# Kernel tuning notes

Hardware: AMD Instinct MI355X
Metric: run time of the kernel (lower is better)

The kernel has to match this reference:

```python
import jax, jax.numpy as jnp
import numpy as np

P_DROP = 0.2
N_NODES = 100000
N_EDGES = 1600000
IN_DIM, HID_DIM, OUT_DIM = 128, 128, 64


def sage_conv(x, src, dst, Wl, Wr, b, n_nodes):
    # PyG SAGEConv (aggr='mean', root_weight=True):
    #   out_i = W_l @ mean_{j in N(i)} x_j + W_r @ x_i + b
    msgs = jnp.take(x, src, axis=0)                                   # [E, d]
    agg = jax.ops.segment_sum(msgs, dst, num_segments=n_nodes)        # [N, d]
    cnt = jax.ops.segment_sum(jnp.ones((src.shape[0],), x.dtype), dst,
                              num_segments=n_nodes)                   # [N]
    agg = agg / jnp.maximum(cnt, 1.0)[:, None]                        # mean, 0 for isolated nodes
    return agg @ Wl + x @ Wr + b


def setup_inputs() -> dict:
    key = jax.random.key(0)
    ks = jax.random.split(key, 8)
    x = jax.random.normal(ks[0], (N_NODES, IN_DIM), dtype=jnp.float32)
    edge_index = jax.random.randint(ks[1], (2, N_EDGES), 0, N_NODES, dtype=jnp.int32)
    drop_u = jax.random.uniform(ks[2], (N_NODES, HID_DIM), dtype=jnp.float32)
    s1 = 1.0 / np.sqrt(IN_DIM)
    s2 = 1.0 / np.sqrt(HID_DIM)
    W1l = jax.random.normal(ks[3], (IN_DIM, HID_DIM), dtype=jnp.float32) * s1
    W1r = jax.random.normal(ks[4], (IN_DIM, HID_DIM), dtype=jnp.float32) * s1
    b1 = jnp.zeros((HID_DIM,), dtype=jnp.float32)
    W2l = jax.random.normal(ks[5], (HID_DIM, OUT_DIM), dtype=jnp.float32) * s2
    W2r = jax.random.normal(ks[6], (HID_DIM, OUT_DIM), dtype=jnp.float32) * s2
    b2 = jnp.zeros((OUT_DIM,), dtype=jnp.float32)
    return {"x": x, "edge_index": edge_index, "drop_u": drop_u,
            "W1l": W1l, "W1r": W1r, "b1": b1,
            "W2l": W2l, "W2r": W2r, "b2": b2}


def reference(x, edge_index, drop_u, W1l, W1r, b1, W2l, W2r, b2):
    n = x.shape[0]
    src, dst = edge_index[0], edge_index[1]
    h = jax.nn.elu(sage_conv(x, src, dst, W1l, W1r, b1, n))
    keep = (drop_u >= P_DROP).astype(h.dtype) / (1.0 - P_DROP)  # inverted dropout, p=0.2
    h = h * keep
    h = jax.nn.elu(sage_conv(h, src, dst, W2l, W2r, b2, n))
    return h
```

## Files before the change

kernel.cpp:

```cpp
#include <hip/hip_runtime.h>
#include <cstdint>
#include <cstddef>

#define TPB 256
#define BCAP 2560
#define NBKMAX 800
#define EPB 8192

typedef short bf16x8 __attribute__((ext_vector_type(8)));
typedef float f32x4 __attribute__((ext_vector_type(4)));

__device__ __forceinline__ unsigned short f2bf(float f) {
  unsigned int u = __float_as_uint(f);
  unsigned int r = (u + 0x7fffu + ((u >> 16) & 1u)) >> 16;
  return (unsigned short)r;
}
__device__ __forceinline__ float bf2f(unsigned short h) {
  return __uint_as_float(((unsigned int)h) << 16);
}

__device__ __forceinline__ void gload16(const void* g, void* l) {
  __builtin_amdgcn_global_load_lds(
      (const __attribute__((address_space(1))) unsigned int*)g,
      (__attribute__((address_space(3))) unsigned int*)l, 16, 0, 0);
}


__global__ __launch_bounds__(256) void multisplit_scatter(
    const int* __restrict__ src, const int* __restrict__ dst,
    unsigned int* __restrict__ be, int* __restrict__ bcnt, int e, int nbk) {
  __shared__ int hist[NBKMAX];
  __shared__ int curs[NBKMAX];
  int tx = threadIdx.x;
  int e0 = blockIdx.x * EPB;
  int e1 = min(e, e0 + EPB);

  for (int b = tx; b < nbk; b += TPB) hist[b] = 0;
  __syncthreads();
  for (int i = e0 + tx; i < e1; i += TPB) atomicAdd(&hist[dst[i] >> 7], 1);
  __syncthreads();
  int rot = (blockIdx.x * 131) % nbk;
  for (int s = tx; s < nbk; s += TPB) {
    int b = s + rot;
    if (b >= nbk) b -= nbk;
    int h = hist[b];
    curs[b] = (h > 0) ? atomicAdd(&bcnt[b], h) : 0;
  }
  __syncthreads();
  for (int i = e0 + tx; i < e1; i += TPB) {
    int d = dst[i];
    int b = d >> 7;
    int p = atomicAdd(&curs[b], 1);
    if (p < BCAP)
      be[(size_t)b * BCAP + p] = ((unsigned int)(d & 127) << 17) | (unsigned int)src[i];
  }
}

__global__ void bucket_scan(const int* __restrict__ bcnt, int* __restrict__ bbase, int nbk) {
  __shared__ int s[TPB];
  __shared__ int carry;
  int tx = threadIdx.x;
  if (tx == 0) carry = 0;
  __syncthreads();
  for (int base = 0; base < nbk; base += TPB) {
    int i = base + tx;
    int v = (i < nbk) ? bcnt[i] : 0;
    s[tx] = v;
    __syncthreads();
    for (int d = 1; d < TPB; d <<= 1) {
      int t = (tx >= d) ? s[tx - d] : 0;
      __syncthreads();
      s[tx] += t;
      __syncthreads();
    }
    int c = carry;
    if (i < nbk) bbase[i] = c + s[tx] - v;
    __syncthreads();
    if (tx == TPB - 1) carry = c + s[tx];
    __syncthreads();
  }
}

__global__ __launch_bounds__(256) void per_bucket_build(
    const unsigned int* __restrict__ be, const int* __restrict__ bcnt,
    const int* __restrict__ bbase, int* __restrict__ off, int* __restrict__ col,
    int n, int e) {
  int b = blockIdx.x, tx = threadIdx.x;
  int cnt = bcnt[b];
  if (cnt > BCAP) cnt = BCAP;
  int base = bbase[b];
  int node0 = b << 7;
  __shared__ int scnt[128];
  __shared__ int sscan[128];
  if (tx < 128) scnt[tx] = 0;
  __syncthreads();
  const unsigned int* eb = be + (size_t)b * BCAP;
  for (int i = tx; i < cnt; i += 256) atomicAdd(&scnt[eb[i] >> 17], 1);
  __syncthreads();
  if (tx < 128) sscan[tx] = scnt[tx];
  __syncthreads();
  for (int d = 1; d < 128; d <<= 1) {
    int t = 0;
    if (tx < 128 && tx >= d) t = sscan[tx - d];
    __syncthreads();
    if (tx < 128) sscan[tx] += t;
    __syncthreads();
  }
  if (tx < 128) {
    int excl = sscan[tx] - scnt[tx];
    if (node0 + tx < n) off[node0 + tx] = base + excl;
    scnt[tx] = excl;
  }
  if (b == 0 && tx == 0) off[n] = e;
  __syncthreads();
  for (int i = tx; i < cnt; i += 256) {
    unsigned int u = eb[i];
    int p = atomicAdd(&scnt[u >> 17], 1);
    col[base + p] = (int)(u & 0x1ffff);
  }
}


__global__ void f32_to_bf16_v4(const float* __restrict__ in, unsigned short* __restrict__ out,
                               int n4) {
  int i = blockIdx.x * TPB + threadIdx.x;
  if (i >= n4) return;
  float4 v = ((const float4*)in)[i];
  ushort4 o;
  o.x = f2bf(v.x); o.y = f2bf(v.y); o.z = f2bf(v.z); o.w = f2bf(v.w);
  ((ushort4*)out)[i] = o;
}

__global__ void make_dropmask(const float* __restrict__ u, unsigned char* __restrict__ m,
                              int n4) {
  int i = blockIdx.x * TPB + threadIdx.x;
  if (i >= n4) return;
  float4 v = ((const float4*)u)[i];
  uchar4 o;
  o.x = (v.x >= 0.2f) ? 1 : 0;
  o.y = (v.y >= 0.2f) ? 1 : 0;
  o.z = (v.z >= 0.2f) ? 1 : 0;
  o.w = (v.w >= 0.2f) ? 1 : 0;
  ((uchar4*)m)[i] = o;
}

template <int NF>
__global__ void build_wt(const float* __restrict__ Wl, const float* __restrict__ Wr,
                         unsigned short* __restrict__ Wt) {
  int idx = blockIdx.x * TPB + threadIdx.x;
  if (idx >= NF * 256) return;
  int nn = idx >> 8;
  int k = idx & 255;
  float v = (k < 128) ? Wl[k * NF + nn] : Wr[(k - 128) * NF + nn];
  Wt[idx] = f2bf(v);
}


__global__ void aggregate_bf(const unsigned short* __restrict__ X,
                             const int* __restrict__ off, const int* __restrict__ col,
                             unsigned short* __restrict__ out, int n) {
  int node = (blockIdx.x * TPB + threadIdx.x) >> 6;
  int lane = threadIdx.x & 63;
  if (node >= n) return;
  int s0 = off[node], s1 = off[node + 1];
  float ax = 0.f, ay = 0.f;
  int e = s0;
  for (; e + 4 <= s1; e += 4) {
    int c0 = col[e], c1 = col[e + 1], c2 = col[e + 2], c3 = col[e + 3];
    unsigned int v0 = *(const unsigned int*)(X + (size_t)c0 * 128 + lane * 2);
    unsigned int v1 = *(const unsigned int*)(X + (size_t)c1 * 128 + lane * 2);
    unsigned int v2 = *(const unsigned int*)(X + (size_t)c2 * 128 + lane * 2);
    unsigned int v3 = *(const unsigned int*)(X + (size_t)c3 * 128 + lane * 2);
    ax += bf2f(v0 & 0xffff) + bf2f(v1 & 0xffff) + bf2f(v2 & 0xffff) + bf2f(v3 & 0xffff);
    ay += bf2f(v0 >> 16) + bf2f(v1 >> 16) + bf2f(v2 >> 16) + bf2f(v3 >> 16);
  }
  for (; e < s1; ++e) {
    int c = col[e];
    unsigned int v = *(const unsigned int*)(X + (size_t)c * 128 + lane * 2);
    ax += bf2f(v & 0xffff);
    ay += bf2f(v >> 16);
  }
  float inv = (s1 > s0) ? 1.0f / (float)(s1 - s0) : 0.f;
  unsigned int o = ((unsigned int)f2bf(ay * inv) << 16) | f2bf(ax * inv);
  *(unsigned int*)(out + (size_t)node * 128 + lane * 2) = o;
}


template <int NT, bool DROP, bool OUT32>
__global__ __launch_bounds__(256) void gemm_mfma(
    const unsigned short* __restrict__ A1, const unsigned short* __restrict__ A2,
    const unsigned short* __restrict__ Wt, const float* __restrict__ bias,
    const unsigned char* __restrict__ dmask, unsigned short* __restrict__ outb,
    float* __restrict__ outf, int n) {
  constexpr int NF = 32 * NT;
  __shared__ __align__(16) unsigned short sA[128 * 64];
  __shared__ __align__(16) unsigned short sB[NF * 64];

  int tid = threadIdx.x;
  int row0 = blockIdx.x * 128;
  int lane = tid & 63;
  int wid = tid >> 6;
  int wm = wid >> 1, wn = wid & 1;
  int lq = lane & 15, q = lane >> 4;

  int sr = tid >> 3, sc8 = tid & 7;
  int cg = sc8 ^ (sr & 7);

  f32x4 acc[4][NT];
#pragma unroll
  for (int i = 0; i < 4; ++i)
#pragma unroll
    for (int j = 0; j < NT; ++j) acc[i][j] = (f32x4)(0.f);

#pragma unroll
  for (int c = 0; c < 4; ++c) {
    const unsigned short* Asrc = (c < 2) ? A1 : A2;
    int koff = (c & 1) * 64;
    if (c > 0) __syncthreads();
#pragma unroll
    for (int t = 0; t < 4; ++t) {
      int row = min(row0 + sr + t * 32, n - 1);
      gload16(Asrc + (size_t)row * 128 + koff + cg * 8,
              (char*)sA + t * 4096 + wid * 1024);
    }
#pragma unroll
    for (int t = 0; t < NT; ++t) {
      gload16(Wt + (size_t)(sr + t * 32) * 256 + c * 64 + cg * 8,
              (char*)sB + t * 4096 + wid * 1024);
    }
    __syncthreads();

#pragma unroll
    for (int ks = 0; ks < 2; ++ks) {
      bf16x8 a[4], b[NT];
#pragma unroll
      for (int i = 0; i < 4; ++i) {
        int rr = wm * 64 + i * 16 + lq;
        a[i] = *(const bf16x8*)(&sA[rr * 64 + (((ks * 4 + q) ^ (rr & 7)) * 8)]);
      }
#pragma unroll
      for (int j = 0; j < NT; ++j) {
        int rb = wn * NT * 16 + j * 16 + lq;
        b[j] = *(const bf16x8*)(&sB[rb * 64 + (((ks * 4 + q) ^ (rb & 7)) * 8)]);
      }
#pragma unroll
      for (int i = 0; i < 4; ++i)
#pragma unroll
        for (int j = 0; j < NT; ++j)
          acc[i][j] = __builtin_amdgcn_mfma_f32_16x16x32_bf16(a[i], b[j], acc[i][j], 0, 0, 0);
    }
  }

#pragma unroll
  for (int j = 0; j < NT; ++j) {
    int colg = wn * NT * 16 + j * 16 + lq;
    float bv = bias[colg];
#pragma unroll
    for (int i = 0; i < 4; ++i) {
      int rbase = row0 + wm * 64 + i * 16 + q * 4;
#pragma unroll
      for (int r = 0; r < 4; ++r) {
        int row = rbase + r;
        if (row >= n) continue;
        float v = acc[i][j][r] + bv;
        v = (v > 0.f) ? v : expm1f(v);
        if (DROP) {
          unsigned char k = dmask[(size_t)row * 128 + colg];
          v = k ? v * 1.25f : 0.f;
        }
        if (OUT32) outf[(size_t)row * NF + colg] = v;
        else outb[(size_t)row * NF + colg] = f2bf(v);
      }
    }
  }
}


extern "C" void kernel_launch(void* const* d_in, const int* in_sizes, int n_in,
                              void* d_out, int out_size, void* d_ws, size_t ws_size,
                              hipStream_t stream) {
  const float* x = (const float*)d_in[0];
  const int* ei = (const int*)d_in[1];
  const float* dropu = (const float*)d_in[2];
  const float* W1l = (const float*)d_in[3];
  const float* W1r = (const float*)d_in[4];
  const float* b1 = (const float*)d_in[5];
  const float* W2l = (const float*)d_in[6];
  const float* W2r = (const float*)d_in[7];
  const float* b2 = (const float*)d_in[8];

  int n = in_sizes[0] / 128;
  int e = in_sizes[1] / 2;
  const int* src = ei;
  const int* dst = ei + e;
  float* out = (float*)d_out;

  char* w = (char*)d_ws;
  auto alloc = [&](size_t bytes) -> char* {
    char* p = w;
    w += (bytes + 255) & ~(size_t)255;
    return p;
  };
  int nbk = (n + 127) / 128;
  int* off = (int*)alloc((size_t)(n + 1) * sizeof(int));
  int* col = (int*)alloc((size_t)e * sizeof(int));
  int* bcnt = (int*)alloc((size_t)nbk * sizeof(int));
  int* bbase = (int*)alloc((size_t)nbk * sizeof(int));
  unsigned short* xb = (unsigned short*)alloc((size_t)n * 128 * 2);
  unsigned short* hb = (unsigned short*)alloc((size_t)n * 128 * 2);
  unsigned short* aggb = (unsigned short*)alloc((size_t)n * 128 * 2);
  unsigned char* dmask = (unsigned char*)alloc((size_t)n * 128);
  unsigned short* Wt1 = (unsigned short*)alloc(128 * 256 * 2);
  unsigned short* Wt2 = (unsigned short*)alloc(64 * 256 * 2);
  unsigned int* be = (unsigned int*)aggb;

  hipMemsetAsync(bcnt, 0, (size_t)nbk * sizeof(int), stream);

  int gMS = (e + EPB - 1) / EPB;
  multisplit_scatter<<<gMS, TPB, 0, stream>>>(src, dst, be, bcnt, e, nbk);
  bucket_scan<<<1, TPB, 0, stream>>>(bcnt, bbase, nbk);
  per_bucket_build<<<nbk, TPB, 0, stream>>>(be, bcnt, bbase, off, col, n, e);

  int n4 = n * 128 / 4;
  f32_to_bf16_v4<<<(n4 + TPB - 1) / TPB, TPB, 0, stream>>>(x, xb, n4);
  make_dropmask<<<(n4 + TPB - 1) / TPB, TPB, 0, stream>>>(dropu, dmask, n4);
  build_wt<128><<<(128 * 256 + TPB - 1) / TPB, TPB, 0, stream>>>(W1l, W1r, Wt1);
  build_wt<64><<<(64 * 256 + TPB - 1) / TPB, TPB, 0, stream>>>(W2l, W2r, Wt2);

  int gN = (n + 3) / 4;
  int gR = (n + 127) / 128;

  aggregate_bf<<<gN, TPB, 0, stream>>>(xb, off, col, aggb, n);
  gemm_mfma<4, true, false><<<gR, TPB, 0, stream>>>(aggb, xb, Wt1, b1, dmask, hb, nullptr, n);

  aggregate_bf<<<gN, TPB, 0, stream>>>(hb, off, col, aggb, n);
  gemm_mfma<2, false, true><<<gR, TPB, 0, stream>>>(aggb, hb, Wt2, b2, nullptr, nullptr, out, n);
}
```

Before: 460.1 us.

## Double-buffer LDS tiles in MFMA GEMM to overlap global loads with compute

The GEMM kernel now keeps two LDS buffers for the A and W tiles. It issues loads for the next K chunks before computing the current one, and uses explicit vmcnt waits and barriers in place of full __syncthreads. This is meant to hide global-to-LDS load latency behind MFMA work. In exchange it doubles LDS usage, which may lower occupancy, and it relies on hand-counted waitcnt values being correct.

```diff
diff --git a/kernel.cpp b/kernel.cpp
--- a/kernel.cpp
+++ b/kernel.cpp
@@ -23,6 +23,11 @@
   __builtin_amdgcn_global_load_lds(
       (const __attribute__((address_space(1))) unsigned int*)g,
       (__attribute__((address_space(3))) unsigned int*)l, 16, 0, 0);
+}
+
+template <int N>
+__device__ __forceinline__ void waitvm() {
+  asm volatile("s_waitcnt vmcnt(%0)" ::"n"(N) : "memory");
 }
 
 
@@ -193,8 +198,9 @@
     const unsigned char* __restrict__ dmask, unsigned short* __restrict__ outb,
     float* __restrict__ outf, int n) {
   constexpr int NF = 32 * NT;
-  __shared__ __align__(16) unsigned short sA[128 * 64];
-  __shared__ __align__(16) unsigned short sB[NF * 64];
+  constexpr int IPC = 4 + NT;
+  __shared__ __align__(16) unsigned short sA[2][128 * 64];
+  __shared__ __align__(16) unsigned short sB[2][NF * 64];
 
   int tid = threadIdx.x;
   int row0 = blockIdx.x * 128;
@@ -206,48 +212,66 @@
   int sr = tid >> 3, sc8 = tid & 7;
   int cg = sc8 ^ (sr & 7);
 
+  int arow[4];
+#pragma unroll
+  for (int t = 0; t < 4; ++t) arow[t] = min(row0 + sr + t * 32, n - 1);
+
   f32x4 acc[4][NT];
 #pragma unroll
   for (int i = 0; i < 4; ++i)
 #pragma unroll
     for (int j = 0; j < NT; ++j) acc[i][j] = (f32x4)(0.f);
 
-#pragma unroll
-  for (int c = 0; c < 4; ++c) {
+  auto issue = [&](int c, int b) {
     const unsigned short* Asrc = (c < 2) ? A1 : A2;
     int koff = (c & 1) * 64;
-    if (c > 0) __syncthreads();
 #pragma unroll
     for (int t = 0; t < 4; ++t) {
-      int row = min(row0 + sr + t * 32, n - 1);
-      gload16(Asrc + (size_t)row * 128 + koff + cg * 8,
-              (char*)sA + t * 4096 + wid * 1024);
+      gload16(Asrc + (size_t)arow[t] * 128 + koff + cg * 8,
+              (char*)sA[b] + t * 4096 + wid * 1024);
     }
 #pragma unroll
     for (int t = 0; t < NT; ++t) {
       gload16(Wt + (size_t)(sr + t * 32) * 256 + c * 64 + cg * 8,
-              (char*)sB + t * 4096 + wid * 1024);
-    }
-    __syncthreads();
-
+              (char*)sB[b] + t * 4096 + wid * 1024);
+    }
+  };
+
+  issue(0, 0);
+  issue(1, 1);
+
+#pragma unroll
+  for (int c = 0; c < 4; ++c) {
+    if (c < 3) waitvm<IPC>(); else waitvm<0>();
+    __builtin_amdgcn_s_barrier();
+    __builtin_amdgcn_sched_barrier(0);
+
+    const int buf = c & 1;
 #pragma unroll
     for (int ks = 0; ks < 2; ++ks) {
       bf16x8 a[4], b[NT];
 #pragma unroll
       for (int i = 0; i < 4; ++i) {
         int rr = wm * 64 + i * 16 + lq;
-        a[i] = *(const bf16x8*)(&sA[rr * 64 + (((ks * 4 + q) ^ (rr & 7)) * 8)]);
+        a[i] = *(const bf16x8*)(&sA[buf][rr * 64 + (((ks * 4 + q) ^ (rr & 7)) * 8)]);
       }
 #pragma unroll
       for (int j = 0; j < NT; ++j) {
         int rb = wn * NT * 16 + j * 16 + lq;
-        b[j] = *(const bf16x8*)(&sB[rb * 64 + (((ks * 4 + q) ^ (rb & 7)) * 8)]);
+        b[j] = *(const bf16x8*)(&sB[buf][rb * 64 + (((ks * 4 + q) ^ (rb & 7)) * 8)]);
       }
 #pragma unroll
       for (int i = 0; i < 4; ++i)
 #pragma unroll
         for (int j = 0; j < NT; ++j)
           acc[i][j] = __builtin_amdgcn_mfma_f32_16x16x32_bf16(a[i], b[j], acc[i][j], 0, 0, 0);
+    }
+
+    if (c < 2) {
+      asm volatile("s_waitcnt lgkmcnt(0)" ::: "memory");
+      __builtin_amdgcn_sched_barrier(0);
+      __builtin_amdgcn_s_barrier();
+      issue(c + 2, buf);
     }
   }
 
```

Result: no change. 454.9 us (-1.1%).
